# Kernel optimization log

Measured on AMD Instinct MI355X. Metric: run time of the kernel, lower is better.

## Reference

```python
import jax, jax.numpy as jnp
import numpy as np

BS, SEQ, DIM, NH = 2, 2048, 2048, 16
HD = DIM // NH  # 128


def setup_inputs() -> dict:
    key = jax.random.key(0)
    ks = jax.random.split(key, 6)
    x = jax.random.normal(ks[0], (BS, SEQ, DIM), dtype=jnp.float32)
    # rotary frequencies, theta=10000 as in LLaMA
    inv_freq = 1.0 / (10000.0 ** (jnp.arange(0, HD, 2, dtype=jnp.float32) / HD))  # [HD/2]
    t = jnp.arange(SEQ, dtype=jnp.float32)
    freqs = jnp.outer(t, inv_freq)  # [SEQ, HD/2]
    freqs_cos = jnp.cos(freqs)
    freqs_sin = jnp.sin(freqs)
    # additive causal mask [1,1,S,S]
    causal = jnp.tril(jnp.ones((SEQ, SEQ), dtype=bool))
    mask = jnp.where(causal, 0.0, -1e9).astype(jnp.float32)[None, None]
    scale = 0.02
    wq = jax.random.normal(ks[1], (DIM, DIM), dtype=jnp.float32) * scale
    wk = jax.random.normal(ks[2], (DIM, DIM), dtype=jnp.float32) * scale
    wv = jax.random.normal(ks[3], (DIM, DIM), dtype=jnp.float32) * scale
    wo = jax.random.normal(ks[4], (DIM, DIM), dtype=jnp.float32) * scale
    return {"x": x, "freqs_cos": freqs_cos, "freqs_sin": freqs_sin, "mask": mask,
            "wq": wq, "wk": wk, "wv": wv, "wo": wo}


def _apply_rope(t, cos, sin):
    # t: [b,s,h,hd]; cos/sin: [s,hd/2]
    tr = t.reshape(*t.shape[:-1], HD // 2, 2)
    tre, tim = tr[..., 0], tr[..., 1]
    c = cos[None, :, None, :]
    s = sin[None, :, None, :]
    out_re = tre * c - tim * s
    out_im = tre * s + tim * c
    return jnp.stack([out_re, out_im], axis=-1).reshape(t.shape)


def reference(x, freqs_cos, freqs_sin, mask, wq, wk, wv, wo):
    bs, seq, _ = x.shape
    q = (x @ wq).reshape(bs, seq, NH, HD)
    k = (x @ wk).reshape(bs, seq, NH, HD)
    v = (x @ wv).reshape(bs, seq, NH, HD)
    q = _apply_rope(q, freqs_cos, freqs_sin)
    k = _apply_rope(k, freqs_cos, freqs_sin)
    # [b,h,s,s]
    scores = jnp.einsum("bqhd,bkhd->bhqk", q, k) / np.sqrt(HD).astype(np.float32)
    scores = scores + mask
    probs = jax.nn.softmax(scores, axis=-1)
    out = jnp.einsum("bhqk,bkhd->bqhd", probs, v).reshape(bs, seq, DIM)
    return out @ wo
```

## Files before the change

kernel.cpp:

```cpp
#include <hip/hip_runtime.h>
#include <hip/hip_bf16.h>
#include <stdint.h>
#include <stddef.h>

#define SEQ 2048
#define DIM 2048
#define NH 16
#define HD 128
#define BSZ 2
#define MTOT (BSZ*SEQ)
#define KDIM DIM

typedef __bf16 bf16;
typedef __attribute__((ext_vector_type(4))) __bf16 bf16x4;
typedef __attribute__((ext_vector_type(8))) __bf16 bf16x8;
typedef __attribute__((ext_vector_type(4))) float f32x4;

#define MFMA16(a,b,c) __builtin_amdgcn_mfma_f32_16x16x32_bf16((a),(b),(c),0,0,0)

__device__ __forceinline__ void glds16(const void* g, void* l) {
  __builtin_amdgcn_global_load_lds((__attribute__((address_space(1))) void*)(g),
                                   (__attribute__((address_space(3))) void*)(l),
                                   16, 0, 0);
}

__device__ __forceinline__ f32x4 f4zero() { f32x4 v = {0.f, 0.f, 0.f, 0.f}; return v; }

__global__ void cast_x_bf16(const float* __restrict__ in, bf16* __restrict__ out) {
  size_t i = (size_t)blockIdx.x * blockDim.x + threadIdx.x;
  float4 v = ((const float4*)in)[i];
  bf16x4 ov;
  ov.x = (bf16)v.x; ov.y = (bf16)v.y; ov.z = (bf16)v.z; ov.w = (bf16)v.w;
  ((bf16x4*)out)[i] = ov;
}

__global__ void transpose_w(const float* __restrict__ W, bf16* __restrict__ WT) {
  __shared__ float tile[64][65];
  const int bk = blockIdx.x, bn = blockIdx.y;
  const int tid = threadIdx.x;
  const int tc = tid & 15, tr = tid >> 4;
#pragma unroll
  for (int p = 0; p < 4; ++p) {
    int k = tr + p * 16;
    float4 v = *(const float4*)(W + (size_t)(bk * 64 + k) * DIM + bn * 64 + tc * 4);
    tile[k][tc * 4 + 0] = v.x;
    tile[k][tc * 4 + 1] = v.y;
    tile[k][tc * 4 + 2] = v.z;
    tile[k][tc * 4 + 3] = v.w;
  }
  __syncthreads();
#pragma unroll
  for (int p = 0; p < 4; ++p) {
    int n = tr + p * 16;
    bf16x4 ov;
    ov.x = (bf16)tile[tc * 4 + 0][n];
    ov.y = (bf16)tile[tc * 4 + 1][n];
    ov.z = (bf16)tile[tc * 4 + 2][n];
    ov.w = (bf16)tile[tc * 4 + 3][n];
    *(bf16x4*)(WT + (size_t)(bn * 64 + n) * DIM + bk * 64 + tc * 4) = ov;
  }
}

template<int EPI>
__global__ __launch_bounds__(256, 2)
void gemm_bf16(const bf16* __restrict__ A, const bf16* __restrict__ BT,
               void* __restrict__ Cout,
               const float* __restrict__ cosT, const float* __restrict__ sinT)
{
  __shared__ __align__(16) bf16 As[2][128 * 32];
  __shared__ __align__(16) bf16 Bs[2][128 * 32];
  const int tid = threadIdx.x;
  const int lane = tid & 63;
  const int w = tid >> 6;
  const int l15 = lane & 15, h4 = lane >> 4;
  const int wr = w >> 1, wc = w & 1;
  const int bn = blockIdx.x, bm = blockIdx.y;
  const int rowA0 = bm * 128, colB0 = bn * 128;

  f32x4 acc[4][4];
#pragma unroll
  for (int m = 0; m < 4; ++m)
#pragma unroll
    for (int n = 0; n < 4; ++n) acc[m][n] = f4zero();

  const uint8_t* Abytes = (const uint8_t*)A;
  const uint8_t* Bbytes = (const uint8_t*)BT;

  auto stage = [&](int buf, int t) {
    const int k0b = t * 64;
#pragma unroll
    for (int j = 0; j < 2; ++j) {
      int chunk = w * 128 + j * 64 + lane;
      int row = chunk >> 2, c = chunk & 3;
      int jj = (c * 16) ^ (((row >> 1) & 3) << 4);
      glds16(Abytes + (size_t)(rowA0 + row) * (KDIM * 2) + k0b + jj,
             (uint8_t*)&As[buf][0] + (w * 128 + j * 64) * 16);
      glds16(Bbytes + (size_t)(colB0 + row) * (KDIM * 2) + k0b + jj,
             (uint8_t*)&Bs[buf][0] + (w * 128 + j * 64) * 16);
    }
  };

  stage(0, 0);
  __syncthreads();

  const int NT = KDIM / 32;
  for (int t = 0; t < NT; ++t) {
    int cur = t & 1;
    if (t + 1 < NT) stage(cur ^ 1, t + 1);
    const uint8_t* Ab = (const uint8_t*)&As[cur][0];
    const uint8_t* Bb = (const uint8_t*)&Bs[cur][0];
    bf16x8 aF[4], bF[4];
#pragma unroll
    for (int m = 0; m < 4; ++m) {
      int row = wr * 64 + m * 16 + l15;
      int off = row * 64 + ((h4 * 16) ^ (((row >> 1) & 3) << 4));
      aF[m] = *(const bf16x8*)(Ab + off);
    }
#pragma unroll
    for (int n = 0; n < 4; ++n) {
      int row = wc * 64 + n * 16 + l15;
      int off = row * 64 + ((h4 * 16) ^ (((row >> 1) & 3) << 4));
      bF[n] = *(const bf16x8*)(Bb + off);
    }
#pragma unroll
    for (int m = 0; m < 4; ++m)
#pragma unroll
      for (int n = 0; n < 4; ++n)
        acc[m][n] = MFMA16(aF[m], bF[n], acc[m][n]);
    __syncthreads();
  }

  const int row0 = rowA0 + wr * 64, col0 = colB0 + wc * 64;
#pragma unroll
  for (int m = 0; m < 4; ++m) {
#pragma unroll
    for (int n = 0; n < 4; ++n) {
#pragma unroll
      for (int r = 0; r < 4; ++r) {
        int row = row0 + m * 16 + h4 * 4 + r;
        int col = col0 + n * 16 + l15;
        float v = acc[m][n][r];
        if constexpr (EPI == 0) {
          ((float*)Cout)[(size_t)row * DIM + col] = v;
        } else if constexpr (EPI == 1) {
          float v2 = __shfl_xor(v, 1);
          int s = row & (SEQ - 1);
          int jidx = (col & (HD - 1)) >> 1;
          float c = cosT[s * (HD / 2) + jidx];
          float sn = sinT[s * (HD / 2) + jidx];
          float o = (col & 1) ? fmaf(v2, sn, v * c) : fmaf(v, c, -(v2 * sn));
          ((bf16*)Cout)[(size_t)row * DIM + col] = (bf16)o;
        } else {
          int hh = col >> 7, d = col & (HD - 1);
          int b = row >> 11, s = row & (SEQ - 1);
          ((bf16*)Cout)[((size_t)(b * NH + hh) * HD + d) * SEQ + s] = (bf16)v;
        }
      }
    }
  }
}

__global__ __launch_bounds__(256, 2)
void flash_attn(const bf16* __restrict__ Q, const bf16* __restrict__ Kg,
                const bf16* __restrict__ VT, bf16* __restrict__ O)
{
  __shared__ __align__(16) bf16 Ks[64 * 128];
  __shared__ __align__(16) bf16 Vs[128 * 64];
  __shared__ __align__(16) bf16 Ps[4][16 * 64];

  const int qt = blockIdx.x, h = blockIdx.y, b = blockIdx.z;
  const int tid = threadIdx.x, lane = tid & 63, w = tid >> 6;
  const int l15 = lane & 15, h4 = lane >> 4;
  const int q0 = qt * 64;

  const bf16* qbase = Q + ((size_t)(b * SEQ + q0 + w * 16 + l15)) * DIM + h * HD;
  bf16x8 aQ[4];
#pragma unroll
  for (int kb = 0; kb < 4; ++kb)
    aQ[kb] = *(const bf16x8*)(qbase + kb * 32 + h4 * 8);

  f32x4 o[8];
#pragma unroll
  for (int i = 0; i < 8; ++i) o[i] = f4zero();
  float mrow[4], lrow[4];
#pragma unroll
  for (int r = 0; r < 4; ++r) { mrow[r] = -1e30f; lrow[r] = 0.0f; }

  const float scale = 0.08838834764831845f;
  const uint8_t* kgb = (const uint8_t*)Kg + ((size_t)(b * SEQ) * DIM + h * HD) * 2;
  const uint8_t* vgb = (const uint8_t*)VT + ((size_t)(b * NH + h) * HD * SEQ) * 2;

  for (int t = 0; t <= qt; ++t) {
    __syncthreads();
    const uint8_t* ksrc = kgb + (size_t)t * 64 * (DIM * 2);
#pragma unroll
    for (int j = 0; j < 4; ++j) {
      int chunk = w * 256 + j * 64 + lane;
      int key = chunk >> 4, c = chunk & 15;
      int jj = (c * 16) ^ ((key & 7) << 4);
      glds16(ksrc + (size_t)key * (DIM * 2) + jj,
             (uint8_t*)Ks + (w * 256 + j * 64) * 16);
    }
    const uint8_t* vsrc = vgb + (size_t)t * 64 * 2;
#pragma unroll
    for (int j = 0; j < 4; ++j) {
      int chunk = w * 256 + j * 64 + lane;
      int d = chunk >> 3, c = chunk & 7;
      int jj = (c * 16) ^ ((d & 7) << 4);
      glds16(vsrc + (size_t)d * (SEQ * 2) + jj,
             (uint8_t*)Vs + (w * 256 + j * 64) * 16);
    }
    __syncthreads();

    f32x4 S[4];
#pragma unroll
    for (int nb = 0; nb < 4; ++nb) {
      f32x4 a = f4zero();
      int key = nb * 16 + l15;
      int swz = (key & 7) << 4;
#pragma unroll
      for (int kb = 0; kb < 4; ++kb) {
        int off = key * 256 + (((kb * 32 + h4 * 8) * 2) ^ swz);
        bf16x8 bK = *(const bf16x8*)((const uint8_t*)Ks + off);
        a = MFMA16(aQ[kb], bK, a);
      }
      S[nb] = a;
    }

    const int qrow0 = q0 + w * 16 + h4 * 4;
    const int key0 = t * 64 + l15;
#pragma unroll
    for (int nb = 0; nb < 4; ++nb)
#pragma unroll
      for (int r = 0; r < 4; ++r) {
        float sv = S[nb][r] * scale;
        if (key0 + nb * 16 > qrow0 + r) sv = -1e9f;
        S[nb][r] = sv;
      }

    float p[4][4];
#pragma unroll
    for (int r = 0; r < 4; ++r) {
      float mx = fmaxf(fmaxf(S[0][r], S[1][r]), fmaxf(S[2][r], S[3][r]));
      mx = fmaxf(mx, __shfl_xor(mx, 1));
      mx = fmaxf(mx, __shfl_xor(mx, 2));
      mx = fmaxf(mx, __shfl_xor(mx, 4));
      mx = fmaxf(mx, __shfl_xor(mx, 8));
      float mnew = fmaxf(mrow[r], mx);
      float corr = __expf(mrow[r] - mnew);
      float s0 = 0.f;
#pragma unroll
      for (int nb = 0; nb < 4; ++nb) {
        float pv = __expf(S[nb][r] - mnew);
        p[nb][r] = pv;
        s0 += pv;
      }
      s0 += __shfl_xor(s0, 1);
      s0 += __shfl_xor(s0, 2);
      s0 += __shfl_xor(s0, 4);
      s0 += __shfl_xor(s0, 8);
      lrow[r] = lrow[r] * corr + s0;
      mrow[r] = mnew;
#pragma unroll
      for (int nb2 = 0; nb2 < 8; ++nb2) o[nb2][r] *= corr;
    }

    uint8_t* pbase = (uint8_t*)&Ps[w][0];
#pragma unroll
    for (int r = 0; r < 4; ++r) {
      int qr = h4 * 4 + r;
      int swz = (qr & 7) << 4;
#pragma unroll
      for (int nb = 0; nb < 4; ++nb) {
        int off = ((qr * 64 + nb * 16 + l15) * 2) ^ swz;
        *(bf16*)(pbase + off) = (bf16)p[nb][r];
      }
    }
    asm volatile("s_waitcnt lgkmcnt(0)" ::: "memory");
    __builtin_amdgcn_sched_barrier(0);

    bf16x8 aP[2];
#pragma unroll
    for (int kb2 = 0; kb2 < 2; ++kb2) {
      int off = ((l15 * 64 + kb2 * 32 + h4 * 8) * 2) ^ ((l15 & 7) << 4);
      aP[kb2] = *(const bf16x8*)(pbase + off);
    }
#pragma unroll
    for (int nb2 = 0; nb2 < 8; ++nb2) {
      int d = nb2 * 16 + l15;
      int swz = (d & 7) << 4;
#pragma unroll
      for (int kb2 = 0; kb2 < 2; ++kb2) {
        int off = d * 128 + (((kb2 * 32 + h4 * 8) * 2) ^ swz);
        bf16x8 bV = *(const bf16x8*)((const uint8_t*)Vs + off);
        o[nb2] = MFMA16(aP[kb2], bV, o[nb2]);
      }
    }
  }

  float inv[4];
#pragma unroll
  for (int r = 0; r < 4; ++r) inv[r] = 1.0f / lrow[r];
  bf16* obase = O + ((size_t)(b * SEQ + q0 + w * 16)) * DIM + h * HD;
#pragma unroll
  for (int nb2 = 0; nb2 < 8; ++nb2)
#pragma unroll
    for (int r = 0; r < 4; ++r)
      obase[(size_t)(h4 * 4 + r) * DIM + nb2 * 16 + l15] = (bf16)(o[nb2][r] * inv[r]);
}

extern "C" void kernel_launch(void* const* d_in, const int* in_sizes, int n_in,
                              void* d_out, int out_size, void* d_ws, size_t ws_size,
                              hipStream_t stream)
{
  const float* x    = (const float*)d_in[0];
  const float* fcos = (const float*)d_in[1];
  const float* fsin = (const float*)d_in[2];
  const float* wq   = (const float*)d_in[4];
  const float* wk   = (const float*)d_in[5];
  const float* wv   = (const float*)d_in[6];
  const float* wo   = (const float*)d_in[7];

  uint8_t* ws = (uint8_t*)d_ws;
  const size_t SZ_XB = (size_t)MTOT * DIM * 2;
  const size_t SZ_WT = (size_t)DIM * DIM * 2;

  bf16* xb    = (bf16*)(ws);
  bf16* wqT   = (bf16*)(ws + SZ_XB);
  bf16* wkT   = (bf16*)(ws + SZ_XB + 1 * SZ_WT);
  bf16* wvT   = (bf16*)(ws + SZ_XB + 2 * SZ_WT);
  bf16* woT   = (bf16*)(ws + SZ_XB + 3 * SZ_WT);
  bf16* qb    = (bf16*)(ws + SZ_XB + 4 * SZ_WT);
  bf16* kb    = (bf16*)(ws + 2 * SZ_XB + 4 * SZ_WT);
  bf16* vT    = (bf16*)(ws + 3 * SZ_XB + 4 * SZ_WT);
  bf16* attnb = xb;

  cast_x_bf16<<<(MTOT * DIM) / (256 * 4), 256, 0, stream>>>(x, xb);
  dim3 tg(DIM / 64, DIM / 64);
  transpose_w<<<tg, 256, 0, stream>>>(wq, wqT);
  transpose_w<<<tg, 256, 0, stream>>>(wk, wkT);
  transpose_w<<<tg, 256, 0, stream>>>(wv, wvT);
  transpose_w<<<tg, 256, 0, stream>>>(wo, woT);

  dim3 gg(DIM / 128, MTOT / 128);
  gemm_bf16<1><<<gg, 256, 0, stream>>>(xb, wqT, qb, fcos, fsin);
  gemm_bf16<1><<<gg, 256, 0, stream>>>(xb, wkT, kb, fcos, fsin);
  gemm_bf16<2><<<gg, 256, 0, stream>>>(xb, wvT, vT, nullptr, nullptr);

  flash_attn<<<dim3(SEQ / 64, NH, BSZ), 256, 0, stream>>>(qb, kb, vT, attnb);

  gemm_bf16<0><<<gg, 256, 0, stream>>>(attnb, woT, (float*)d_out, nullptr, nullptr);
}
```

Baseline: 508.2 us.

## Double-buffer K/V, pair causal q-tiles, compute S transposed with register P

Rewrites the flash attention kernel so each block handles two mirrored query tiles (pr and last-pr), which balances causal work across blocks and halves the grid. K/V tiles are double-buffered in LDS, and the next tile is prefetched while the current one is computed. S is computed as K·Q^T so the softmax row reduction becomes a cross-lane shuffle, and P is repacked in registers via shuffles instead of going through an LDS round-trip. Masking is applied only on the diagonal tile, and s_setprio is used around the MFMA sections; the cost is twice the LDS and more register pressure, which may lower occupancy.

Measured after the change: 440.3 us. 13.4% less time.

```diff
diff --git a/kernel.cpp b/kernel.cpp
--- a/kernel.cpp
+++ b/kernel.cpp
@@ -25,6 +25,12 @@
 }
 
 __device__ __forceinline__ f32x4 f4zero() { f32x4 v = {0.f, 0.f, 0.f, 0.f}; return v; }
+
+__device__ __forceinline__ uint32_t bpack(float a, float b) {
+  uint16_t au = __builtin_bit_cast(uint16_t, (bf16)a);
+  uint16_t bu = __builtin_bit_cast(uint16_t, (bf16)b);
+  return (uint32_t)au | ((uint32_t)bu << 16);
+}
 
 __global__ void cast_x_bf16(const float* __restrict__ in, bf16* __restrict__ out) {
   size_t i = (size_t)blockIdx.x * blockDim.x + threadIdx.x;
@@ -164,149 +170,171 @@
 void flash_attn(const bf16* __restrict__ Q, const bf16* __restrict__ Kg,
                 const bf16* __restrict__ VT, bf16* __restrict__ O)
 {
-  __shared__ __align__(16) bf16 Ks[64 * 128];
-  __shared__ __align__(16) bf16 Vs[128 * 64];
-  __shared__ __align__(16) bf16 Ps[4][16 * 64];
-
-  const int qt = blockIdx.x, h = blockIdx.y, b = blockIdx.z;
+  __shared__ __align__(16) bf16 Ks[2][64 * 128];
+  __shared__ __align__(16) bf16 Vs[2][128 * 64];
+
+  const int pr = blockIdx.x, h = blockIdx.y, b = blockIdx.z;
   const int tid = threadIdx.x, lane = tid & 63, w = tid >> 6;
   const int l15 = lane & 15, h4 = lane >> 4;
-  const int q0 = qt * 64;
-
-  const bf16* qbase = Q + ((size_t)(b * SEQ + q0 + w * 16 + l15)) * DIM + h * HD;
-  bf16x8 aQ[4];
-#pragma unroll
-  for (int kb = 0; kb < 4; ++kb)
-    aQ[kb] = *(const bf16x8*)(qbase + kb * 32 + h4 * 8);
-
-  f32x4 o[8];
-#pragma unroll
-  for (int i = 0; i < 8; ++i) o[i] = f4zero();
-  float mrow[4], lrow[4];
-#pragma unroll
-  for (int r = 0; r < 4; ++r) { mrow[r] = -1e30f; lrow[r] = 0.0f; }
+  const bool hhalf = ((h4 >> 1) & 1) != 0;
 
   const float scale = 0.08838834764831845f;
   const uint8_t* kgb = (const uint8_t*)Kg + ((size_t)(b * SEQ) * DIM + h * HD) * 2;
   const uint8_t* vgb = (const uint8_t*)VT + ((size_t)(b * NH + h) * HD * SEQ) * 2;
 
-  for (int t = 0; t <= qt; ++t) {
-    __syncthreads();
+  auto stageKV = [&](int buf, int t) {
     const uint8_t* ksrc = kgb + (size_t)t * 64 * (DIM * 2);
+    const uint8_t* vsrc = vgb + (size_t)t * 64 * 2;
 #pragma unroll
     for (int j = 0; j < 4; ++j) {
       int chunk = w * 256 + j * 64 + lane;
-      int key = chunk >> 4, c = chunk & 15;
-      int jj = (c * 16) ^ ((key & 7) << 4);
-      glds16(ksrc + (size_t)key * (DIM * 2) + jj,
-             (uint8_t*)Ks + (w * 256 + j * 64) * 16);
-    }
-    const uint8_t* vsrc = vgb + (size_t)t * 64 * 2;
-#pragma unroll
-    for (int j = 0; j < 4; ++j) {
-      int chunk = w * 256 + j * 64 + lane;
-      int d = chunk >> 3, c = chunk & 7;
-      int jj = (c * 16) ^ ((d & 7) << 4);
-      glds16(vsrc + (size_t)d * (SEQ * 2) + jj,
-             (uint8_t*)Vs + (w * 256 + j * 64) * 16);
-    }
+      int key = chunk >> 4, ck = chunk & 15;
+      int jk = (ck * 16) ^ ((key & 7) << 4);
+      glds16(ksrc + (size_t)key * (DIM * 2) + jk,
+             (uint8_t*)&Ks[buf][0] + (w * 256 + j * 64) * 16);
+      int d = chunk >> 3, cv = chunk & 7;
+      int jv = (cv * 16) ^ ((d & 7) << 4);
+      glds16(vsrc + (size_t)d * (SEQ * 2) + jv,
+             (uint8_t*)&Vs[buf][0] + (w * 256 + j * 64) * 16);
+    }
+  };
+
+#pragma unroll 1
+  for (int qsel = 0; qsel < 2; ++qsel) {
+    const int qt = qsel ? (SEQ / 64 - 1 - pr) : pr;
+    const int q0 = qt * 64;
+    const int qrow = q0 + w * 16 + l15;
+
+    const bf16* qbase = Q + ((size_t)(b * SEQ + qrow)) * DIM + h * HD;
+    bf16x8 aQ[4];
+#pragma unroll
+    for (int kk = 0; kk < 4; ++kk)
+      aQ[kk] = *(const bf16x8*)(qbase + kk * 32 + h4 * 8);
+
+    f32x4 o[8];
+#pragma unroll
+    for (int i = 0; i < 8; ++i) o[i] = f4zero();
+    float mrun = -1e30f, lrun = 0.0f;
+
+    stageKV(0, 0);
     __syncthreads();
 
-    f32x4 S[4];
-#pragma unroll
-    for (int nb = 0; nb < 4; ++nb) {
-      f32x4 a = f4zero();
-      int key = nb * 16 + l15;
-      int swz = (key & 7) << 4;
+#pragma unroll 1
+    for (int t = 0; t <= qt; ++t) {
+      const int cur = t & 1;
+      if (t < qt) stageKV(cur ^ 1, t + 1);
+
+      f32x4 S[4];
+      __builtin_amdgcn_s_setprio(1);
 #pragma unroll
       for (int kb = 0; kb < 4; ++kb) {
-        int off = key * 256 + (((kb * 32 + h4 * 8) * 2) ^ swz);
-        bf16x8 bK = *(const bf16x8*)((const uint8_t*)Ks + off);
-        a = MFMA16(aQ[kb], bK, a);
-      }
-      S[nb] = a;
-    }
-
-    const int qrow0 = q0 + w * 16 + h4 * 4;
-    const int key0 = t * 64 + l15;
-#pragma unroll
-    for (int nb = 0; nb < 4; ++nb)
-#pragma unroll
-      for (int r = 0; r < 4; ++r) {
-        float sv = S[nb][r] * scale;
-        if (key0 + nb * 16 > qrow0 + r) sv = -1e9f;
-        S[nb][r] = sv;
-      }
-
-    float p[4][4];
-#pragma unroll
-    for (int r = 0; r < 4; ++r) {
-      float mx = fmaxf(fmaxf(S[0][r], S[1][r]), fmaxf(S[2][r], S[3][r]));
-      mx = fmaxf(mx, __shfl_xor(mx, 1));
-      mx = fmaxf(mx, __shfl_xor(mx, 2));
-      mx = fmaxf(mx, __shfl_xor(mx, 4));
-      mx = fmaxf(mx, __shfl_xor(mx, 8));
-      float mnew = fmaxf(mrow[r], mx);
-      float corr = __expf(mrow[r] - mnew);
-      float s0 = 0.f;
-#pragma unroll
-      for (int nb = 0; nb < 4; ++nb) {
-        float pv = __expf(S[nb][r] - mnew);
-        p[nb][r] = pv;
-        s0 += pv;
-      }
-      s0 += __shfl_xor(s0, 1);
-      s0 += __shfl_xor(s0, 2);
-      s0 += __shfl_xor(s0, 4);
-      s0 += __shfl_xor(s0, 8);
-      lrow[r] = lrow[r] * corr + s0;
-      mrow[r] = mnew;
-#pragma unroll
-      for (int nb2 = 0; nb2 < 8; ++nb2) o[nb2][r] *= corr;
-    }
-
-    uint8_t* pbase = (uint8_t*)&Ps[w][0];
-#pragma unroll
-    for (int r = 0; r < 4; ++r) {
-      int qr = h4 * 4 + r;
-      int swz = (qr & 7) << 4;
-#pragma unroll
-      for (int nb = 0; nb < 4; ++nb) {
-        int off = ((qr * 64 + nb * 16 + l15) * 2) ^ swz;
-        *(bf16*)(pbase + off) = (bf16)p[nb][r];
-      }
-    }
-    asm volatile("s_waitcnt lgkmcnt(0)" ::: "memory");
-    __builtin_amdgcn_sched_barrier(0);
-
-    bf16x8 aP[2];
-#pragma unroll
-    for (int kb2 = 0; kb2 < 2; ++kb2) {
-      int off = ((l15 * 64 + kb2 * 32 + h4 * 8) * 2) ^ ((l15 & 7) << 4);
-      aP[kb2] = *(const bf16x8*)(pbase + off);
-    }
-#pragma unroll
-    for (int nb2 = 0; nb2 < 8; ++nb2) {
-      int d = nb2 * 16 + l15;
-      int swz = (d & 7) << 4;
+        f32x4 a = f4zero();
+        int key = kb * 16 + l15;
+        int swz = (key & 7) << 4;
+#pragma unroll
+        for (int kk = 0; kk < 4; ++kk) {
+          bf16x8 aK = *(const bf16x8*)((const uint8_t*)&Ks[cur][0] + key * 256 +
+                                       (((kk * 32 + h4 * 8) * 2) ^ swz));
+          a = MFMA16(aK, aQ[kk], a);
+        }
+        S[kb] = a;
+      }
+      __builtin_amdgcn_s_setprio(0);
+
+      if (t == qt) {
+#pragma unroll
+        for (int kb = 0; kb < 4; ++kb)
+#pragma unroll
+          for (int r = 0; r < 4; ++r) {
+            int key = q0 + kb * 16 + h4 * 4 + r;
+            float sv = S[kb][r] * scale;
+            S[kb][r] = (key > qrow) ? -1e9f : sv;
+          }
+      } else {
+#pragma unroll
+        for (int kb = 0; kb < 4; ++kb)
+#pragma unroll
+          for (int r = 0; r < 4; ++r) S[kb][r] *= scale;
+      }
+
+      float pmax = S[0][0];
+#pragma unroll
+      for (int kb = 0; kb < 4; ++kb)
+#pragma unroll
+        for (int r = 0; r < 4; ++r) pmax = fmaxf(pmax, S[kb][r]);
+      pmax = fmaxf(pmax, __shfl_xor(pmax, 16));
+      pmax = fmaxf(pmax, __shfl_xor(pmax, 32));
+      float mnew = fmaxf(mrun, pmax);
+      float corr = __expf(mrun - mnew);
+      float p[4][4];
+      float psum = 0.f;
+#pragma unroll
+      for (int kb = 0; kb < 4; ++kb)
+#pragma unroll
+        for (int r = 0; r < 4; ++r) {
+          float pv = __expf(S[kb][r] - mnew);
+          p[kb][r] = pv;
+          psum += pv;
+        }
+      psum += __shfl_xor(psum, 16);
+      psum += __shfl_xor(psum, 32);
+      lrun = lrun * corr + psum;
+      mrun = mnew;
+#pragma unroll
+      for (int i = 0; i < 8; ++i) o[i] *= corr;
+
+      uint32_t pk[4][2];
+#pragma unroll
+      for (int kb = 0; kb < 4; ++kb) {
+        pk[kb][0] = bpack(p[kb][0], p[kb][1]);
+        pk[kb][1] = bpack(p[kb][2], p[kb][3]);
+      }
+
+      bf16x8 pB[2];
 #pragma unroll
       for (int kb2 = 0; kb2 < 2; ++kb2) {
-        int off = d * 128 + (((kb2 * 32 + h4 * 8) * 2) ^ swz);
-        bf16x8 bV = *(const bf16x8*)((const uint8_t*)Vs + off);
-        o[nb2] = MFMA16(aP[kb2], bV, o[nb2]);
-      }
-    }
-  }
-
-  float inv[4];
-#pragma unroll
-  for (int r = 0; r < 4; ++r) inv[r] = 1.0f / lrow[r];
-  bf16* obase = O + ((size_t)(b * SEQ + q0 + w * 16)) * DIM + h * HD;
-#pragma unroll
-  for (int nb2 = 0; nb2 < 8; ++nb2)
-#pragma unroll
-    for (int r = 0; r < 4; ++r)
-      obase[(size_t)(h4 * 4 + r) * DIM + nb2 * 16 + l15] = (bf16)(o[nb2][r] * inv[r]);
+        uint32_t s0a = hhalf ? pk[kb2 * 2 + 1][0] : pk[kb2 * 2][0];
+        uint32_t s0b = hhalf ? pk[kb2 * 2 + 1][1] : pk[kb2 * 2][1];
+        uint32_t s1a = hhalf ? pk[kb2 * 2][0] : pk[kb2 * 2 + 1][0];
+        uint32_t s1b = hhalf ? pk[kb2 * 2][1] : pk[kb2 * 2 + 1][1];
+        uint32_t e16a = __shfl_xor(s0a, 16), e16b = __shfl_xor(s0b, 16);
+        uint32_t e32a = __shfl_xor(s1a, 32), e32b = __shfl_xor(s1b, 32);
+        uint32_t e48a = __shfl_xor(s1a, 48), e48b = __shfl_xor(s1b, 48);
+        uint32_t lo0 = (h4 == 0) ? s0a : (h4 == 1) ? e48a : (h4 == 2) ? e32a : e16a;
+        uint32_t lo1 = (h4 == 0) ? s0b : (h4 == 1) ? e48b : (h4 == 2) ? e32b : e16b;
+        uint32_t hi0 = (h4 == 0) ? e16a : (h4 == 1) ? e32a : (h4 == 2) ? e48a : s0a;
+        uint32_t hi1 = (h4 == 0) ? e16b : (h4 == 1) ? e32b : (h4 == 2) ? e48b : s0b;
+        uint4 u = make_uint4(lo0, lo1, hi0, hi1);
+        pB[kb2] = __builtin_bit_cast(bf16x8, u);
+      }
+
+      __builtin_amdgcn_s_setprio(1);
+#pragma unroll
+      for (int db = 0; db < 8; ++db) {
+        int drow = db * 16 + l15;
+        int swz = (drow & 7) << 4;
+#pragma unroll
+        for (int kb2 = 0; kb2 < 2; ++kb2) {
+          bf16x8 aV = *(const bf16x8*)((const uint8_t*)&Vs[cur][0] + drow * 128 +
+                                       (((kb2 * 32 + h4 * 8) * 2) ^ swz));
+          o[db] = MFMA16(aV, pB[kb2], o[db]);
+        }
+      }
+      __builtin_amdgcn_s_setprio(0);
+
+      __syncthreads();
+    }
+
+    float inv = 1.0f / lrun;
+    bf16* obase = O + ((size_t)(b * SEQ + qrow)) * DIM + h * HD;
+#pragma unroll
+    for (int db = 0; db < 8; ++db) {
+      uint32_t w0 = bpack(o[db][0] * inv, o[db][1] * inv);
+      uint32_t w1 = bpack(o[db][2] * inv, o[db][3] * inv);
+      uint2 st = make_uint2(w0, w1);
+      *(uint2*)(obase + db * 16 + h4 * 4) = st;
+    }
+  }
 }
 
 extern "C" void kernel_launch(void* const* d_in, const int* in_sizes, int n_in,
@@ -347,7 +375,7 @@
   gemm_bf16<1><<<gg, 256, 0, stream>>>(xb, wkT, kb, fcos, fsin);
   gemm_bf16<2><<<gg, 256, 0, stream>>>(xb, wvT, vT, nullptr, nullptr);
 
-  flash_attn<<<dim3(SEQ / 64, NH, BSZ), 256, 0, stream>>>(qb, kb, vT, attnb);
+  flash_attn<<<dim3(SEQ / 128, NH, BSZ), 256, 0, stream>>>(qb, kb, vT, attnb);
 
   gemm_bf16<0><<<gg, 256, 0, stream>>>(attnb, woT, (float*)d_out, nullptr, nullptr);
 }
```
